# Kernel optimization log

Hardware: AMD Instinct MI355X
Metric: run time of the kernel (lower is better)

Reference implementation:

```python
import jax, jax.numpy as jnp
import numpy as np

D_MODEL = 2048
H_PER_EXPERT = 1408
NUM_EXPERTS = 8
NUM_TOKENS = 8192
TOP_K = 2
SCORE_SCALE_FACTOR = 1.0


def setup_inputs() -> dict:
    key = jax.random.key(0)
    kx, kr, ks, kg, ku, kd = jax.random.split(key, 6)
    x = jax.random.normal(kx, (NUM_TOKENS, D_MODEL), dtype=jnp.float32)
    # Balanced routing: each expert receives exactly NUM_TOKENS*TOP_K/NUM_EXPERTS slots,
    # so per-expert split sizes are equal (static) and no tokens are dropped.
    slots = NUM_TOKENS * TOP_K
    flat = jnp.tile(jnp.arange(NUM_EXPERTS, dtype=jnp.int32), slots // NUM_EXPERTS)
    topK_indices = jax.random.permutation(kr, flat).reshape(NUM_TOKENS, TOP_K)
    topK_scores = jax.random.uniform(ks, (NUM_TOKENS, TOP_K), dtype=jnp.float32)
    scale = 0.02
    W_gate = scale * jax.random.normal(kg, (NUM_EXPERTS, D_MODEL, H_PER_EXPERT), dtype=jnp.float32)
    W_up = scale * jax.random.normal(ku, (NUM_EXPERTS, D_MODEL, H_PER_EXPERT), dtype=jnp.float32)
    W_down = scale * jax.random.normal(kd, (NUM_EXPERTS, H_PER_EXPERT, D_MODEL), dtype=jnp.float32)
    return {"x": x, "topK_indices": topK_indices, "topK_scores": topK_scores,
            "W_gate": W_gate, "W_up": W_up, "W_down": W_down}


def reference(x, topK_indices, topK_scores, W_gate, W_up, W_down):
    E = W_gate.shape[0]
    B, k = topK_indices.shape
    slots = B * k
    cap = slots // E  # equal per-expert batch size (balanced routing)

    flat_idx = topK_indices.reshape(-1)          # [slots]
    flat_scores = topK_scores.reshape(-1)        # [slots]
    batch_idx = jnp.repeat(jnp.arange(B, dtype=flat_idx.dtype), k)  # [slots]

    order = jnp.argsort(flat_idx, stable=True)   # sort slots by expert id
    sorted_scores = flat_scores[order]
    sorted_batch = batch_idx[order]

    # Dispatch: gather token features, group per expert -> [E, cap, d]
    xs = x[sorted_batch].reshape(E, cap, -1)

    # Per-expert GLU MLP as grouped GEMMs
    gate = jax.nn.silu(jnp.einsum('ecd,edh->ech', xs, W_gate))
    up = jnp.einsum('ecd,edh->ech', xs, W_up)
    down = jnp.einsum('ech,ehd->ecd', gate * up, W_down).reshape(slots, -1)

    # Gate-score scaling and scatter-add combine
    down = down * (sorted_scores[:, None] * SCORE_SCALE_FACTOR)
    y = jax.ops.segment_sum(down, sorted_batch, num_segments=B)
    return y
```

## Files before the change

### kernel.cpp

```cpp
#include <hip/hip_runtime.h>
#include <stdint.h>

#define NUM_TOKENS 8192
#define D_MODEL    2048
#define H_EXP      1408
#define NUM_EXP    8
#define TOPK       2
#define N_SLOTS    (NUM_TOKENS * TOPK)
#define CAP        (N_SLOTS / NUM_EXP)

typedef __attribute__((ext_vector_type(4))) float f32x4;
typedef __attribute__((ext_vector_type(8))) short short8_t;

__device__ __forceinline__ unsigned short f2bf(float f) {
    unsigned u = __float_as_uint(f);
    u += 0x7FFFu + ((u >> 16) & 1u);
    return (unsigned short)(u >> 16);
}
__device__ __forceinline__ float bf2f(unsigned short h) {
    return __uint_as_float(((unsigned)h) << 16);
}
__device__ __forceinline__ void async_ld16(const void* g, void* l) {
    __builtin_amdgcn_global_load_lds(
        (const __attribute__((address_space(1))) void*)g,
        (__attribute__((address_space(3))) void*)l,
        16, 0, 0);
}

__global__ void route_kernel(const int* __restrict__ topk_idx,
                             const float* __restrict__ topk_scr,
                             int* __restrict__ src_token,
                             float* __restrict__ src_score,
                             int* __restrict__ pos_of_slot) {
    const int e = blockIdx.x;
    const int tid = threadIdx.x;
    const int lane = tid & 63;
    const int wv = tid >> 6;
    __shared__ int wave_tot[4];
    __shared__ int base_s;
    if (tid == 0) base_s = 0;
    __syncthreads();
    for (int t0 = 0; t0 < N_SLOTS; t0 += 256) {
        const int s = t0 + tid;
        const bool m = (topk_idx[s] == e);
        const unsigned long long bal = __ballot(m);
        const int prefix = __popcll(bal & ((1ull << lane) - 1ull));
        if (lane == 0) wave_tot[wv] = __popcll(bal);
        __syncthreads();
        int wbase = 0;
        #pragma unroll
        for (int w = 0; w < 4; ++w) if (w < wv) wbase += wave_tot[w];
        const int btot = wave_tot[0] + wave_tot[1] + wave_tot[2] + wave_tot[3];
        if (m) {
            const int p = e * CAP + base_s + wbase + prefix;
            src_token[p] = s >> 1;
            src_score[p] = topk_scr[s];
            pos_of_slot[s] = p;
        }
        __syncthreads();
        if (tid == 0) base_s += btot;
        __syncthreads();
    }
}

__global__ void transpose_cast_kernel(const float* __restrict__ in,
                                      unsigned short* __restrict__ out,
                                      int R, int C) {
    __shared__ float tile[32][33];
    const int c0 = blockIdx.x * 32;
    const int r0 = blockIdx.y * 32;
    const float* inp = in + (size_t)blockIdx.z * R * C;
    unsigned short* outp = out + (size_t)blockIdx.z * R * C;
    const int lr = threadIdx.x >> 3;
    const int lc = (threadIdx.x & 7) * 4;
    const float4 v = *(const float4*)(inp + (size_t)(r0 + lr) * C + c0 + lc);
    tile[lr][lc + 0] = v.x;
    tile[lr][lc + 1] = v.y;
    tile[lr][lc + 2] = v.z;
    tile[lr][lc + 3] = v.w;
    __syncthreads();
    ushort4 o;
    o.x = f2bf(tile[lc + 0][lr]);
    o.y = f2bf(tile[lc + 1][lr]);
    o.z = f2bf(tile[lc + 2][lr]);
    o.w = f2bf(tile[lc + 3][lr]);
    *(ushort4*)(outp + (size_t)(c0 + lr) * R + r0 + lc) = o;
}

__global__ void gather_cast_kernel(const float* __restrict__ x,
                                   const int* __restrict__ src_token,
                                   unsigned short* __restrict__ xs) {
    const int p = blockIdx.x;
    const int t = src_token[p];
    const float4* src = (const float4*)(x + (size_t)t * D_MODEL);
    ushort4* dst = (ushort4*)(xs + (size_t)p * D_MODEL);
    for (int i = threadIdx.x; i < D_MODEL / 4; i += 256) {
        const float4 v = src[i];
        ushort4 o;
        o.x = f2bf(v.x); o.y = f2bf(v.y); o.z = f2bf(v.z); o.w = f2bf(v.w);
        dst[i] = o;
    }
}

__global__ void __launch_bounds__(256, 2)
gemm12_kernel(const unsigned short* __restrict__ xs,
              const unsigned short* __restrict__ Wgt,
              const unsigned short* __restrict__ Wut,
              unsigned short* __restrict__ hbuf) {
    __shared__ unsigned short As[128 * 32];
    __shared__ unsigned short Bgs[128 * 32];
    __shared__ unsigned short Bus[128 * 32];

    const int tid = threadIdx.x;
    const int lane = tid & 63;
    const int wv = tid >> 6;
    const int wm = wv & 1;
    const int wn = wv >> 1;
    const int quad = lane >> 4;
    const int l15 = lane & 15;

    const int mt = blockIdx.x;
    const int nt = blockIdx.y;
    const int e  = blockIdx.z;

    const size_t arow0 = (size_t)e * CAP + (size_t)mt * 128;
    const unsigned short* Ag  = xs + arow0 * D_MODEL;
    const unsigned short* Bgg = Wgt + ((size_t)e * H_EXP + (size_t)nt * 128) * D_MODEL;
    const unsigned short* Bug = Wut + ((size_t)e * H_EXP + (size_t)nt * 128) * D_MODEL;

    const int s1 = tid, s2 = tid + 256;
    const int r1 = s1 >> 2, c1 = (s1 & 3) * 8;
    const int r2 = s2 >> 2, c2 = (s2 & 3) * 8;

    const f32x4 zero4 = {0.0f, 0.0f, 0.0f, 0.0f};
    f32x4 accg[4][4], accu[4][4];
    #pragma unroll
    for (int i = 0; i < 4; i++)
        #pragma unroll
        for (int j = 0; j < 4; j++) { accg[i][j] = zero4; accu[i][j] = zero4; }

    for (int k0 = 0; k0 < D_MODEL; k0 += 32) {
        async_ld16(Ag  + (size_t)r1 * D_MODEL + k0 + c1, As  + s1 * 8);
        async_ld16(Ag  + (size_t)r2 * D_MODEL + k0 + c2, As  + s2 * 8);
        async_ld16(Bgg + (size_t)r1 * D_MODEL + k0 + c1, Bgs + s1 * 8);
        async_ld16(Bgg + (size_t)r2 * D_MODEL + k0 + c2, Bgs + s2 * 8);
        async_ld16(Bug + (size_t)r1 * D_MODEL + k0 + c1, Bus + s1 * 8);
        async_ld16(Bug + (size_t)r2 * D_MODEL + k0 + c2, Bus + s2 * 8);
        __syncthreads();

        short8_t af[4], bg[4], bu[4];
        #pragma unroll
        for (int mi = 0; mi < 4; mi++)
            af[mi] = *(const short8_t*)(As + (wm * 64 + mi * 16 + l15) * 32 + quad * 8);
        #pragma unroll
        for (int ni = 0; ni < 4; ni++) {
            bg[ni] = *(const short8_t*)(Bgs + (wn * 64 + ni * 16 + l15) * 32 + quad * 8);
            bu[ni] = *(const short8_t*)(Bus + (wn * 64 + ni * 16 + l15) * 32 + quad * 8);
        }
        #pragma unroll
        for (int mi = 0; mi < 4; mi++)
            #pragma unroll
            for (int ni = 0; ni < 4; ni++) {
                accg[mi][ni] = __builtin_amdgcn_mfma_f32_16x16x32_bf16(af[mi], bg[ni], accg[mi][ni], 0, 0, 0);
                accu[mi][ni] = __builtin_amdgcn_mfma_f32_16x16x32_bf16(af[mi], bu[ni], accu[mi][ni], 0, 0, 0);
            }
        __syncthreads();
    }

    #pragma unroll
    for (int mi = 0; mi < 4; mi++) {
        #pragma unroll
        for (int r = 0; r < 4; r++) {
            const size_t grow = arow0 + (size_t)(wm * 64 + mi * 16 + quad * 4 + r);
            unsigned short* dst = hbuf + grow * H_EXP + (size_t)nt * 128 + wn * 64 + l15;
            #pragma unroll
            for (int ni = 0; ni < 4; ni++) {
                const float g = accg[mi][ni][r];
                const float u = accu[mi][ni][r];
                const float h = (g * u) / (1.0f + __expf(-g));
                dst[ni * 16] = f2bf(h);
            }
        }
    }
}

__global__ void __launch_bounds__(256, 2)
gemm3_kernel(const unsigned short* __restrict__ hbuf,
             const unsigned short* __restrict__ Wdt,
             const float* __restrict__ src_score,
             unsigned short* __restrict__ dbuf) {
    __shared__ unsigned short As[128 * 32];
    __shared__ unsigned short Bs[128 * 32];

    const int tid = threadIdx.x;
    const int lane = tid & 63;
    const int wv = tid >> 6;
    const int wm = wv & 1;
    const int wn = wv >> 1;
    const int quad = lane >> 4;
    const int l15 = lane & 15;

    const int mt = blockIdx.x;
    const int nt = blockIdx.y;
    const int e  = blockIdx.z;

    const size_t arow0 = (size_t)e * CAP + (size_t)mt * 128;
    const unsigned short* Ag = hbuf + arow0 * H_EXP;
    const unsigned short* Bg = Wdt + ((size_t)e * D_MODEL + (size_t)nt * 128) * H_EXP;

    const int s1 = tid, s2 = tid + 256;
    const int r1 = s1 >> 2, c1 = (s1 & 3) * 8;
    const int r2 = s2 >> 2, c2 = (s2 & 3) * 8;

    const f32x4 zero4 = {0.0f, 0.0f, 0.0f, 0.0f};
    f32x4 acc[4][4];
    #pragma unroll
    for (int i = 0; i < 4; i++)
        #pragma unroll
        for (int j = 0; j < 4; j++) acc[i][j] = zero4;

    for (int k0 = 0; k0 < H_EXP; k0 += 32) {
        async_ld16(Ag + (size_t)r1 * H_EXP + k0 + c1, As + s1 * 8);
        async_ld16(Ag + (size_t)r2 * H_EXP + k0 + c2, As + s2 * 8);
        async_ld16(Bg + (size_t)r1 * H_EXP + k0 + c1, Bs + s1 * 8);
        async_ld16(Bg + (size_t)r2 * H_EXP + k0 + c2, Bs + s2 * 8);
        __syncthreads();

        short8_t af[4], bf[4];
        #pragma unroll
        for (int mi = 0; mi < 4; mi++)
            af[mi] = *(const short8_t*)(As + (wm * 64 + mi * 16 + l15) * 32 + quad * 8);
        #pragma unroll
        for (int ni = 0; ni < 4; ni++)
            bf[ni] = *(const short8_t*)(Bs + (wn * 64 + ni * 16 + l15) * 32 + quad * 8);
        #pragma unroll
        for (int mi = 0; mi < 4; mi++)
            #pragma unroll
            for (int ni = 0; ni < 4; ni++)
                acc[mi][ni] = __builtin_amdgcn_mfma_f32_16x16x32_bf16(af[mi], bf[ni], acc[mi][ni], 0, 0, 0);
        __syncthreads();
    }

    #pragma unroll
    for (int mi = 0; mi < 4; mi++) {
        #pragma unroll
        for (int r = 0; r < 4; r++) {
            const size_t grow = arow0 + (size_t)(wm * 64 + mi * 16 + quad * 4 + r);
            const float sc = src_score[grow];
            unsigned short* dst = dbuf + grow * D_MODEL + (size_t)nt * 128 + wn * 64 + l15;
            #pragma unroll
            for (int ni = 0; ni < 4; ni++)
                dst[ni * 16] = f2bf(acc[mi][ni][r] * sc);
        }
    }
}

__global__ void combine_kernel(const unsigned short* __restrict__ dbuf,
                               const int* __restrict__ pos_of_slot,
                               float* __restrict__ y) {
    const int t = blockIdx.x;
    const int p0 = pos_of_slot[2 * t];
    const int p1 = pos_of_slot[2 * t + 1];
    const ushort4* a = (const ushort4*)(dbuf + (size_t)p0 * D_MODEL);
    const ushort4* b = (const ushort4*)(dbuf + (size_t)p1 * D_MODEL);
    float4* o = (float4*)(y + (size_t)t * D_MODEL);
    for (int i = threadIdx.x; i < D_MODEL / 4; i += 256) {
        const ushort4 ua = a[i];
        const ushort4 ub = b[i];
        float4 v;
        v.x = bf2f(ua.x) + bf2f(ub.x);
        v.y = bf2f(ua.y) + bf2f(ub.y);
        v.z = bf2f(ua.z) + bf2f(ub.z);
        v.w = bf2f(ua.w) + bf2f(ub.w);
        o[i] = v;
    }
}

extern "C" void kernel_launch(void* const* d_in, const int* in_sizes, int n_in,
                              void* d_out, int out_size, void* d_ws, size_t ws_size,
                              hipStream_t stream) {
    const float* x        = (const float*)d_in[0];
    const int*   topk_idx = (const int*)d_in[1];
    const float* topk_scr = (const float*)d_in[2];
    const float* Wg       = (const float*)d_in[3];
    const float* Wu       = (const float*)d_in[4];
    const float* Wd       = (const float*)d_in[5];
    float* y = (float*)d_out;

    char* ws = (char*)d_ws;
    const size_t wbytes = (size_t)NUM_EXP * D_MODEL * H_EXP * 2;
    size_t off = 0;
    unsigned short* buf0 = (unsigned short*)(ws + off); off += wbytes;
    unsigned short* Wut  = (unsigned short*)(ws + off); off += wbytes;
    unsigned short* hb   = (unsigned short*)(ws + off); off += wbytes;
    unsigned short* xs   = (unsigned short*)(ws + off); off += (size_t)N_SLOTS * D_MODEL * 2;
    int*   src_token = (int*)(ws + off);   off += (size_t)N_SLOTS * 4;
    float* src_score = (float*)(ws + off); off += (size_t)N_SLOTS * 4;
    int*   pos_slot  = (int*)(ws + off);   off += (size_t)N_SLOTS * 4;
    unsigned short* Wgt  = buf0;
    unsigned short* Wdt  = buf0;
    unsigned short* dbuf = xs;

    route_kernel<<<NUM_EXP, 256, 0, stream>>>(topk_idx, topk_scr, src_token, src_score, pos_slot);
    transpose_cast_kernel<<<dim3(H_EXP / 32, D_MODEL / 32, NUM_EXP), 256, 0, stream>>>(Wg, Wgt, D_MODEL, H_EXP);
    transpose_cast_kernel<<<dim3(H_EXP / 32, D_MODEL / 32, NUM_EXP), 256, 0, stream>>>(Wu, Wut, D_MODEL, H_EXP);
    gather_cast_kernel<<<N_SLOTS, 256, 0, stream>>>(x, src_token, xs);
    gemm12_kernel<<<dim3(CAP / 128, H_EXP / 128, NUM_EXP), 256, 0, stream>>>(xs, Wgt, Wut, hb);
    transpose_cast_kernel<<<dim3(D_MODEL / 32, H_EXP / 32, NUM_EXP), 256, 0, stream>>>(Wd, Wdt, H_EXP, D_MODEL);
    gemm3_kernel<<<dim3(CAP / 128, D_MODEL / 128, NUM_EXP), 256, 0, stream>>>(hb, Wdt, src_score, dbuf);
    combine_kernel<<<NUM_TOKENS, 256, 0, stream>>>(dbuf, pos_slot, y);
}
```

Before: 776.4 us.

## Rework gate/up GEMM into double-buffered 256x128 tile with swizzled LDS

```diff
diff --git a/kernel.cpp b/kernel.cpp
--- a/kernel.cpp
+++ b/kernel.cpp
@@ -8,6 +8,7 @@
 #define TOPK       2
 #define N_SLOTS    (NUM_TOKENS * TOPK)
 #define CAP        (N_SLOTS / NUM_EXP)
+#define KT12       (D_MODEL / 64)
 
 typedef __attribute__((ext_vector_type(4))) float f32x4;
 typedef __attribute__((ext_vector_type(8))) short short8_t;
@@ -102,35 +103,67 @@
     }
 }
 
-__global__ void __launch_bounds__(256, 2)
+#define STAGE_U(ldsbase, src, stride, k0)                                        \
+    async_ld16((src) + (size_t)rA * (stride) + (k0) + gA * 8, (ldsbase) + tid * 8); \
+    async_ld16((src) + (size_t)rB * (stride) + (k0) + gA * 8, (ldsbase) + (tid + 512) * 8);
+
+#define READ_B(dstf, matoff, njbase)                                             \
+    _Pragma("unroll")                                                            \
+    for (int nj = 0; nj < 2; ++nj) {                                             \
+        _Pragma("unroll")                                                        \
+        for (int ks = 0; ks < 2; ++ks) {                                         \
+            const int rr = brow + (njbase + nj) * 16;                            \
+            dstf[nj][ks] = *(const short8_t*)(cb + (matoff) + rr * 64 +          \
+                               (((ks * 4 + quad) ^ (rr & 7)) * 8));              \
+        }                                                                        \
+    }
+
+#define MFMA_BLK(acc, bfr, njbase)                                               \
+    _Pragma("unroll")                                                            \
+    for (int mi = 0; mi < 4; ++mi) {                                             \
+        _Pragma("unroll")                                                        \
+        for (int nj = 0; nj < 2; ++nj) {                                         \
+            _Pragma("unroll")                                                    \
+            for (int ks = 0; ks < 2; ++ks)                                       \
+                acc[mi][(njbase) + nj] = __builtin_amdgcn_mfma_f32_16x16x32_bf16( \
+                    af[mi][ks], bfr[nj][ks], acc[mi][(njbase) + nj], 0, 0, 0);   \
+        }                                                                        \
+    }
+
+#define BAR()    __builtin_amdgcn_s_barrier()
+#define LGKM0()  do { asm volatile("s_waitcnt lgkmcnt(0)" ::: "memory");         \
+                      __builtin_amdgcn_sched_barrier(0); } while (0)
+
+__global__ void __launch_bounds__(512, 2)
 gemm12_kernel(const unsigned short* __restrict__ xs,
               const unsigned short* __restrict__ Wgt,
               const unsigned short* __restrict__ Wut,
               unsigned short* __restrict__ hbuf) {
-    __shared__ unsigned short As[128 * 32];
-    __shared__ unsigned short Bgs[128 * 32];
-    __shared__ unsigned short Bus[128 * 32];
-
-    const int tid = threadIdx.x;
+    __shared__ unsigned short lds[2][512 * 64];
+
+    const int tid  = threadIdx.x;
     const int lane = tid & 63;
-    const int wv = tid >> 6;
-    const int wm = wv & 1;
-    const int wn = wv >> 1;
+    const int wv   = tid >> 6;
+    const int wm   = wv & 3;
+    const int wn   = wv >> 2;
     const int quad = lane >> 4;
-    const int l15 = lane & 15;
+    const int l15  = lane & 15;
 
     const int mt = blockIdx.x;
     const int nt = blockIdx.y;
     const int e  = blockIdx.z;
 
-    const size_t arow0 = (size_t)e * CAP + (size_t)mt * 128;
-    const unsigned short* Ag  = xs + arow0 * D_MODEL;
+    const size_t arow0 = (size_t)e * CAP + (size_t)mt * 256;
+    const unsigned short* Ag  = xs  + arow0 * D_MODEL;
     const unsigned short* Bgg = Wgt + ((size_t)e * H_EXP + (size_t)nt * 128) * D_MODEL;
     const unsigned short* Bug = Wut + ((size_t)e * H_EXP + (size_t)nt * 128) * D_MODEL;
 
-    const int s1 = tid, s2 = tid + 256;
-    const int r1 = s1 >> 2, c1 = (s1 & 3) * 8;
-    const int r2 = s2 >> 2, c2 = (s2 & 3) * 8;
+    const int rA = tid >> 3;
+    const int rB = rA + 64;
+    const int gA = (tid & 7) ^ (rA & 7);
+
+    const int arow = wm * 64 + l15;
+    const int brow = wn * 64 + l15;
 
     const f32x4 zero4 = {0.0f, 0.0f, 0.0f, 0.0f};
     f32x4 accg[4][4], accu[4][4];
@@ -139,52 +172,87 @@
         #pragma unroll
         for (int j = 0; j < 4; j++) { accg[i][j] = zero4; accu[i][j] = zero4; }
 
-    for (int k0 = 0; k0 < D_MODEL; k0 += 32) {
-        async_ld16(Ag  + (size_t)r1 * D_MODEL + k0 + c1, As  + s1 * 8);
-        async_ld16(Ag  + (size_t)r2 * D_MODEL + k0 + c2, As  + s2 * 8);
-        async_ld16(Bgg + (size_t)r1 * D_MODEL + k0 + c1, Bgs + s1 * 8);
-        async_ld16(Bgg + (size_t)r2 * D_MODEL + k0 + c2, Bgs + s2 * 8);
-        async_ld16(Bug + (size_t)r1 * D_MODEL + k0 + c1, Bus + s1 * 8);
-        async_ld16(Bug + (size_t)r2 * D_MODEL + k0 + c2, Bus + s2 * 8);
-        __syncthreads();
-
-        short8_t af[4], bg[4], bu[4];
-        #pragma unroll
-        for (int mi = 0; mi < 4; mi++)
-            af[mi] = *(const short8_t*)(As + (wm * 64 + mi * 16 + l15) * 32 + quad * 8);
-        #pragma unroll
-        for (int ni = 0; ni < 4; ni++) {
-            bg[ni] = *(const short8_t*)(Bgs + (wn * 64 + ni * 16 + l15) * 32 + quad * 8);
-            bu[ni] = *(const short8_t*)(Bus + (wn * 64 + ni * 16 + l15) * 32 + quad * 8);
+    {
+        unsigned short* nb = &lds[0][0];
+        STAGE_U(nb +     0, Ag,                         D_MODEL, 0);
+        STAGE_U(nb +  8192, Ag + (size_t)128 * D_MODEL, D_MODEL, 0);
+        STAGE_U(nb + 16384, Bgg,                        D_MODEL, 0);
+        STAGE_U(nb + 24576, Bug,                        D_MODEL, 0);
+    }
+    asm volatile("s_waitcnt vmcnt(2)" ::: "memory");
+    BAR();
+
+    for (int t = 0; t < KT12; ++t) {
+        const unsigned short* cb = &lds[t & 1][0];
+        unsigned short* nb = &lds[(t + 1) & 1][0];
+        const int k1 = (t + 1) * 64;
+        const bool st = (t + 1) < KT12;
+
+        short8_t af[4][2], b2[2][2];
+
+        #pragma unroll
+        for (int mi = 0; mi < 4; ++mi) {
+            #pragma unroll
+            for (int ks = 0; ks < 2; ++ks) {
+                const int rr = arow + mi * 16;
+                af[mi][ks] = *(const short8_t*)(cb + rr * 64 +
+                                 (((ks * 4 + quad) ^ (rr & 7)) * 8));
+            }
         }
-        #pragma unroll
-        for (int mi = 0; mi < 4; mi++)
-            #pragma unroll
-            for (int ni = 0; ni < 4; ni++) {
-                accg[mi][ni] = __builtin_amdgcn_mfma_f32_16x16x32_bf16(af[mi], bg[ni], accg[mi][ni], 0, 0, 0);
-                accu[mi][ni] = __builtin_amdgcn_mfma_f32_16x16x32_bf16(af[mi], bu[ni], accu[mi][ni], 0, 0, 0);
-            }
-        __syncthreads();
+        READ_B(b2, 16384, 0);
+        if (st) { STAGE_U(nb + 0, Ag, D_MODEL, k1); }
+        BAR(); LGKM0();
+        __builtin_amdgcn_s_setprio(1);
+        MFMA_BLK(accg, b2, 0);
+        __builtin_amdgcn_s_setprio(0);
+        BAR();
+
+        READ_B(b2, 16384, 2);
+        if (st) { STAGE_U(nb + 8192, Ag + (size_t)128 * D_MODEL, D_MODEL, k1); }
+        BAR(); LGKM0();
+        __builtin_amdgcn_s_setprio(1);
+        MFMA_BLK(accg, b2, 2);
+        __builtin_amdgcn_s_setprio(0);
+        if (st) asm volatile("s_waitcnt vmcnt(4)" ::: "memory");
+        else    asm volatile("s_waitcnt vmcnt(0)" ::: "memory");
+        BAR();
+
+        READ_B(b2, 24576, 0);
+        if (st) { STAGE_U(nb + 16384, Bgg, D_MODEL, k1); }
+        BAR(); LGKM0();
+        __builtin_amdgcn_s_setprio(1);
+        MFMA_BLK(accu, b2, 0);
+        __builtin_amdgcn_s_setprio(0);
+        BAR();
+
+        READ_B(b2, 24576, 2);
+        if (st) { STAGE_U(nb + 24576, Bug, D_MODEL, k1); }
+        BAR(); LGKM0();
+        __builtin_amdgcn_s_setprio(1);
+        MFMA_BLK(accu, b2, 2);
+        __builtin_amdgcn_s_setprio(0);
+        asm volatile("s_waitcnt vmcnt(2)" ::: "memory");
+        BAR();
     }
 
     #pragma unroll
-    for (int mi = 0; mi < 4; mi++) {
-        #pragma unroll
-        for (int r = 0; r < 4; r++) {
+    for (int mi = 0; mi < 4; ++mi) {
+        #pragma unroll
+        for (int r = 0; r < 4; ++r) {
             const size_t grow = arow0 + (size_t)(wm * 64 + mi * 16 + quad * 4 + r);
             unsigned short* dst = hbuf + grow * H_EXP + (size_t)nt * 128 + wn * 64 + l15;
             #pragma unroll
-            for (int ni = 0; ni < 4; ni++) {
-                const float g = accg[mi][ni][r];
-                const float u = accu[mi][ni][r];
+            for (int nj = 0; nj < 4; ++nj) {
+                const float g = accg[mi][nj][r];
+                const float u = accu[mi][nj][r];
                 const float h = (g * u) / (1.0f + __expf(-g));
-                dst[ni * 16] = f2bf(h);
+                dst[nj * 16] = f2bf(h);
             }
         }
     }
 }
 
-__global__ void __launch_bounds__(256, 2)
+__global__ void __launch_bounds__(256, 3)
 gemm3_kernel(const unsigned short* __restrict__ hbuf,
              const unsigned short* __restrict__ Wdt,
              const float* __restrict__ src_score,
@@ -305,7 +373,7 @@
     transpose_cast_kernel<<<dim3(H_EXP / 32, D_MODEL / 32, NUM_EXP), 256, 0, stream>>>(Wg, Wgt, D_MODEL, H_EXP);
     transpose_cast_kernel<<<dim3(H_EXP / 32, D_MODEL / 32, NUM_EXP), 256, 0, stream>>>(Wu, Wut, D_MODEL, H_EXP);
     gather_cast_kernel<<<N_SLOTS, 256, 0, stream>>>(x, src_token, xs);
-    gemm12_kernel<<<dim3(CAP / 128, H_EXP / 128, NUM_EXP), 256, 0, stream>>>(xs, Wgt, Wut, hb);
+    gemm12_kernel<<<dim3(CAP / 256, H_EXP / 128, NUM_EXP), 512, 0, stream>>>(xs, Wgt, Wut, hb);
     transpose_cast_kernel<<<dim3(D_MODEL / 32, H_EXP / 32, NUM_EXP), 256, 0, stream>>>(Wd, Wdt, H_EXP, D_MODEL);
     gemm3_kernel<<<dim3(CAP / 128, D_MODEL / 128, NUM_EXP), 256, 0, stream>>>(hb, Wdt, src_score, dbuf);
     combine_kernel<<<NUM_TOKENS, 256, 0, stream>>>(dbuf, pos_slot, y);
```

New measurement: 718.8 us. -7.4%, faster.
